# Performance work log

Measured on AMD Instinct MI355X. Metric: run time of the kernel, lower is better.

Reference implementation:

```python
import jax, jax.numpy as jnp
import numpy as np

NS, NP, EJ, ER = 10000, 2048, 32768, 32768  # skills, job/resume pairs, edges
D, H = 1536, 8
NEG_SLOPE_ATT = 0.2   # GAT attention leaky_relu
NEG_SLOPE = 0.01      # F.leaky_relu / nn.LeakyReLU default


def setup_inputs() -> dict:
    key = jax.random.key(0)
    ks = jax.random.split(key, 20)
    rn = lambda k, shp, s=1.0: jax.random.normal(k, shp, dtype=jnp.float32) * s
    s_d = 1.0 / np.sqrt(D)
    return {
        "x_skill": rn(ks[0], (NS, D)),
        "x_job": rn(ks[1], (NP, D)),
        "x_resume": rn(ks[2], (NP, D)),
        # GraphConv params (lin_rel has bias, lin_root bias=False in PyG)
        "W_rel": rn(ks[3], (D, D), s_d),
        "b_rel": jnp.zeros((D,), jnp.float32),
        "W_root": rn(ks[4], (D, D), s_d),
        # GATConv params (heads=8, concat=False)
        "W_gat_src": rn(ks[5], (D, H * D), s_d),
        "W_gat_dst": rn(ks[6], (D, H * D), s_d),
        "att_src": rn(ks[7], (H, D), s_d),
        "att_dst": rn(ks[8], (H, D), s_d),
        "b_gat": jnp.zeros((D,), jnp.float32),
        # MLP: [3072 -> 512 -> 128 -> 1]
        "W1": rn(ks[9], (2 * D, 512), 1.0 / np.sqrt(2 * D)),
        "b1": jnp.zeros((512,), jnp.float32),
        "W2": rn(ks[10], (512, 128), 1.0 / np.sqrt(512)),
        "b2": jnp.zeros((128,), jnp.float32),
        "W3": rn(ks[11], (128, 1), 1.0 / np.sqrt(128)),
        "b3": jnp.zeros((1,), jnp.float32),
        # edge lists (src = skill idx, dst = job/resume idx)
        "edge_src_job": jax.random.randint(ks[12], (EJ,), 0, NS, dtype=jnp.int32),
        "edge_dst_job": jax.random.randint(ks[13], (EJ,), 0, NP, dtype=jnp.int32),
        "edge_src_res": jax.random.randint(ks[14], (ER,), 0, NS, dtype=jnp.int32),
        "edge_dst_res": jax.random.randint(ks[15], (ER,), 0, NP, dtype=jnp.int32),
    }


def reference(x_skill, x_job, x_resume, W_rel, b_rel, W_root,
              W_gat_src, W_gat_dst, att_src, att_dst, b_gat,
              W1, b1, W2, b2, W3, b3,
              edge_src_job, edge_dst_job, edge_src_res, edge_dst_res):
    n_pair = x_job.shape[0]

    # --- GraphConv (skill -> job): sum-aggregate then linear + root ---
    agg = jax.ops.segment_sum(x_skill[edge_src_job], edge_dst_job,
                              num_segments=n_pair)                  # [NP, D]
    h_job = agg @ W_rel + b_rel + x_job @ W_root                     # [NP, D]

    # --- GATConv (skill -> resume), heads=H, concat=False, no self-loops ---
    xs = (x_skill @ W_gat_src).reshape(-1, H, D)                     # [NS, H, D]
    xd = (x_resume @ W_gat_dst).reshape(-1, H, D)                    # [NP, H, D]
    a_src = jnp.einsum('nhd,hd->nh', xs, att_src)                    # [NS, H]
    a_dst = jnp.einsum('nhd,hd->nh', xd, att_dst)                    # [NP, H]
    e = jax.nn.leaky_relu(a_src[edge_src_res] + a_dst[edge_dst_res],
                          NEG_SLOPE_ATT)                             # [E, H]
    # segment softmax over edges grouped by destination resume node
    e_max = jax.ops.segment_max(e, edge_dst_res, num_segments=n_pair)
    e_exp = jnp.exp(e - e_max[edge_dst_res])
    denom = jax.ops.segment_sum(e_exp, edge_dst_res, num_segments=n_pair)
    alpha = e_exp / (denom[edge_dst_res] + 1e-16)                    # [E, H]
    msg = xs[edge_src_res] * alpha[:, :, None]                       # [E, H, D]
    out = jax.ops.segment_sum(msg, edge_dst_res, num_segments=n_pair)  # [NP, H, D]
    h_res = out.mean(axis=1) + b_gat                                 # concat=False -> head mean

    # --- combine + MLP ---
    h = jnp.concatenate([jax.nn.leaky_relu(h_job, NEG_SLOPE),
                         jax.nn.leaky_relu(h_res, NEG_SLOPE)], axis=1)  # [NP, 2D]
    h = jax.nn.leaky_relu(h @ W1 + b1, NEG_SLOPE)
    h = jax.nn.leaky_relu(h @ W2 + b2, NEG_SLOPE)
    score = (h @ W3 + b3).squeeze(-1)                                # [NP]
    return score, alpha
```

## Files before the change

### kernel.cpp

```cpp
#include <hip/hip_runtime.h>

#define D_ 1536
#define H_ 8

typedef __attribute__((ext_vector_type(8))) short bf16x8;
typedef __attribute__((ext_vector_type(4))) float f32x4;

__device__ __forceinline__ unsigned short f2bf(float f) {
    unsigned u = __builtin_bit_cast(unsigned, f);
    unsigned r = (u + 0x7fffu + ((u >> 16) & 1u)) >> 16;
    return (unsigned short)r;
}

__device__ __forceinline__ unsigned pack2bf(float a, float b) {
    return (unsigned)f2bf(a) | ((unsigned)f2bf(b) << 16);
}

__device__ __forceinline__ float bflo(unsigned u) { return __builtin_bit_cast(float, u << 16); }
__device__ __forceinline__ float bfhi(unsigned u) { return __builtin_bit_cast(float, u & 0xffff0000u); }

__device__ __forceinline__ void gload16(const void* g, void* l) {
    __builtin_amdgcn_global_load_lds((const __attribute__((address_space(1))) void*)g,
                                     (__attribute__((address_space(3))) void*)l, 16, 0, 0);
}

__global__ __launch_bounds__(256) void k_vmat(const float* __restrict__ Wsrc,
                                              const float* __restrict__ Wdst,
                                              const float* __restrict__ att_s,
                                              const float* __restrict__ att_d,
                                              float* __restrict__ Vsrc,
                                              float* __restrict__ Vdst) {
    int id = blockIdx.x;
    int sel = id >= (D_ * H_);
    int idx = sel ? id - D_ * H_ : id;
    int d = idx >> 3, h = idx & 7;
    const float* W = (sel ? Wdst : Wsrc) + (size_t)d * (H_ * D_) + (size_t)h * D_;
    const float* at = (sel ? att_d : att_s) + (size_t)h * D_;
    float s = 0.f;
    for (int i = threadIdx.x; i < D_; i += 256) s += W[i] * at[i];
    for (int o = 32; o; o >>= 1) s += __shfl_down(s, o);
    __shared__ float red[4];
    if ((threadIdx.x & 63) == 0) red[threadIdx.x >> 6] = s;
    __syncthreads();
    if (threadIdx.x == 0) (sel ? Vdst : Vsrc)[d * H_ + h] = red[0] + red[1] + red[2] + red[3];
}

__global__ __launch_bounds__(256) void k_a(const float* __restrict__ x,
                                           const float* __restrict__ V,
                                           float* __restrict__ out, int N) {
    int n = blockIdx.x;
    if (n >= N) return;
    float part[H_] = {};
    const float* xr = x + (size_t)n * D_;
    #pragma unroll
    for (int j = 0; j < 6; j++) {
        int d = threadIdx.x + j * 256;
        float xv = xr[d];
        const float* vp = V + d * H_;
        #pragma unroll
        for (int h = 0; h < H_; h++) part[h] += xv * vp[h];
    }
    __shared__ float red[4][H_];
    int lane = threadIdx.x & 63, w = threadIdx.x >> 6;
    #pragma unroll
    for (int h = 0; h < H_; h++) {
        float v = part[h];
        for (int o = 32; o; o >>= 1) v += __shfl_down(v, o);
        if (lane == 0) red[w][h] = v;
    }
    __syncthreads();
    if (threadIdx.x < H_)
        out[(size_t)n * H_ + threadIdx.x] =
            red[0][threadIdx.x] + red[1][threadIdx.x] + red[2][threadIdx.x] + red[3][threadIdx.x];
}

__global__ void k_count(const int* __restrict__ dj, int ej, const int* __restrict__ dr, int er,
                        int* cnt_j, int* cnt_r) {
    int i = blockIdx.x * blockDim.x + threadIdx.x;
    if (i < ej) atomicAdd(&cnt_j[dj[i]], 1);
    else if (i < ej + er) atomicAdd(&cnt_r[dr[i - ej]], 1);
}

__global__ void k_scan(const int* __restrict__ cnt_j, int* off_j,
                       const int* __restrict__ cnt_r, int* off_r, int NP) {
    const int* cnt = blockIdx.x ? cnt_r : cnt_j;
    int* off = blockIdx.x ? off_r : off_j;
    int lane = threadIdx.x;
    int chunk = (NP + 63) / 64;
    int base = lane * chunk;
    int sum = 0;
    for (int i = 0; i < chunk; i++) { int idx = base + i; if (idx < NP) sum += cnt[idx]; }
    int incl = sum;
    for (int o = 1; o < 64; o <<= 1) { int t = __shfl_up(incl, o); if (lane >= o) incl += t; }
    int run = incl - sum;
    for (int i = 0; i < chunk; i++) { int idx = base + i; if (idx < NP) { off[idx] = run; run += cnt[idx]; } }
    if (lane == 63) off[NP] = run;
}

__global__ void k_scatter(const int* __restrict__ dj, int ej, const int* __restrict__ dr, int er,
                          const int* __restrict__ off_j, int* fill_j, int* sid_j,
                          const int* __restrict__ off_r, int* fill_r, int* sid_r) {
    int i = blockIdx.x * blockDim.x + threadIdx.x;
    if (i < ej) {
        int p = dj[i];
        int slot = atomicAdd(&fill_j[p], 1);
        sid_j[off_j[p] + slot] = i;
    } else if (i < ej + er) {
        int e = i - ej;
        int p = dr[e];
        int slot = atomicAdd(&fill_r[p], 1);
        sid_r[off_r[p] + slot] = e;
    }
}

__global__ __launch_bounds__(256) void k_xsb(const float* __restrict__ x, unsigned* __restrict__ xb) {
    int p = blockIdx.x;
    const float2* xr = (const float2*)x + (size_t)p * 768 + threadIdx.x;
    unsigned* o = xb + (size_t)p * 768 + threadIdx.x;
    #pragma unroll
    for (int j = 0; j < 3; j++) { float2 v = xr[j * 256]; o[j * 256] = pack2bf(v.x, v.y); }
}

__global__ __launch_bounds__(256) void k_agg(const unsigned* __restrict__ xb, const int* __restrict__ src,
                                             const int* __restrict__ sid, const int* __restrict__ cnt,
                                             const int* __restrict__ off, unsigned* __restrict__ cat_u) {
    int p = blockIdx.x;
    int n = cnt[p], o = off[p];
    float2 acc[3] = {};
    int i = 0;
    for (; i + 2 <= n; i += 2) {
        int e0 = sid[o + i], e1 = sid[o + i + 1];
        const unsigned* r0 = xb + (size_t)src[e0] * 768 + threadIdx.x;
        const unsigned* r1 = xb + (size_t)src[e1] * 768 + threadIdx.x;
        unsigned v0[3], v1[3];
        #pragma unroll
        for (int j = 0; j < 3; j++) { v0[j] = r0[j * 256]; v1[j] = r1[j * 256]; }
        #pragma unroll
        for (int j = 0; j < 3; j++) {
            acc[j].x += bflo(v0[j]) + bflo(v1[j]);
            acc[j].y += bfhi(v0[j]) + bfhi(v1[j]);
        }
    }
    if (i < n) {
        int e0 = sid[o + i];
        const unsigned* r0 = xb + (size_t)src[e0] * 768 + threadIdx.x;
        #pragma unroll
        for (int j = 0; j < 3; j++) { unsigned v = r0[j * 256]; acc[j].x += bflo(v); acc[j].y += bfhi(v); }
    }
    unsigned* orow = cat_u + (size_t)p * 1536 + threadIdx.x;
    #pragma unroll
    for (int j = 0; j < 3; j++) orow[j * 256] = pack2bf(acc[j].x, acc[j].y);
}

__global__ __launch_bounds__(256) void k_xjob(const float* __restrict__ x_job,
                                              unsigned* __restrict__ cat_u) {
    int p = blockIdx.x;
    const float2* xr = (const float2*)x_job + (size_t)p * 768 + threadIdx.x;
    unsigned* orow = cat_u + (size_t)p * 1536 + 768 + threadIdx.x;
    #pragma unroll
    for (int j = 0; j < 3; j++) { float2 v = xr[j * 256]; orow[j * 256] = pack2bf(v.x, v.y); }
}

__global__ void k_softmax(const float* __restrict__ a_src, const float* __restrict__ a_dst,
                          const int* __restrict__ src, const int* __restrict__ sid,
                          const int* __restrict__ cnt, const int* __restrict__ off,
                          float* __restrict__ alpha_out) {
    int p = blockIdx.x;
    int n = cnt[p], o = off[p];
    if (n == 0) return;
    int lane = threadIdx.x;
    #pragma unroll 1
    for (int h = 0; h < H_; h++) {
        float ad = a_dst[(size_t)p * H_ + h];
        float m = -3.4e38f;
        for (int i = lane; i < n; i += 64) {
            int e = sid[o + i];
            float v = a_src[(size_t)src[e] * H_ + h] + ad;
            v = v >= 0.f ? v : 0.2f * v;
            m = fmaxf(m, v);
        }
        for (int o2 = 32; o2; o2 >>= 1) m = fmaxf(m, __shfl_xor(m, o2));
        float s = 0.f;
        for (int i = lane; i < n; i += 64) {
            int e = sid[o + i];
            float v = a_src[(size_t)src[e] * H_ + h] + ad;
            v = v >= 0.f ? v : 0.2f * v;
            s += expf(v - m);
        }
        for (int o2 = 32; o2; o2 >>= 1) s += __shfl_xor(s, o2);
        float inv = 1.f / (s + 1e-16f);
        for (int i = lane; i < n; i += 64) {
            int e = sid[o + i];
            float v = a_src[(size_t)src[e] * H_ + h] + ad;
            v = v >= 0.f ? v : 0.2f * v;
            alpha_out[(size_t)e * H_ + h] = expf(v - m) * inv;
        }
    }
}

__global__ __launch_bounds__(256) void k_aggatt(const unsigned* __restrict__ xb,
                                                const float* __restrict__ alpha,
                                                const int* __restrict__ src, const int* __restrict__ sid,
                                                const int* __restrict__ cnt, const int* __restrict__ off,
                                                unsigned* __restrict__ aggatt_u) {
    int p = blockIdx.x;
    int n = cnt[p], o = off[p];
    float2 acc[H_][3] = {};
    int i = 0;
    for (; i + 2 <= n; i += 2) {
        int e0 = sid[o + i], e1 = sid[o + i + 1];
        const unsigned* r0 = xb + (size_t)src[e0] * 768 + threadIdx.x;
        const unsigned* r1 = xb + (size_t)src[e1] * 768 + threadIdx.x;
        unsigned v0[3], v1[3];
        #pragma unroll
        for (int j = 0; j < 3; j++) { v0[j] = r0[j * 256]; v1[j] = r1[j * 256]; }
        const float* a0 = alpha + (size_t)e0 * H_;
        const float* a1 = alpha + (size_t)e1 * H_;
        float f0[3][2], f1[3][2];
        #pragma unroll
        for (int j = 0; j < 3; j++) {
            f0[j][0] = bflo(v0[j]); f0[j][1] = bfhi(v0[j]);
            f1[j][0] = bflo(v1[j]); f1[j][1] = bfhi(v1[j]);
        }
        #pragma unroll
        for (int h = 0; h < H_; h++) {
            float w0 = a0[h], w1 = a1[h];
            #pragma unroll
            for (int j = 0; j < 3; j++) {
                acc[h][j].x += w0 * f0[j][0] + w1 * f1[j][0];
                acc[h][j].y += w0 * f0[j][1] + w1 * f1[j][1];
            }
        }
    }
    if (i < n) {
        int e0 = sid[o + i];
        const unsigned* r0 = xb + (size_t)src[e0] * 768 + threadIdx.x;
        unsigned v0[3];
        #pragma unroll
        for (int j = 0; j < 3; j++) v0[j] = r0[j * 256];
        const float* a0 = alpha + (size_t)e0 * H_;
        #pragma unroll
        for (int h = 0; h < H_; h++) {
            float w0 = a0[h];
            #pragma unroll
            for (int j = 0; j < 3; j++) {
                acc[h][j].x += w0 * bflo(v0[j]);
                acc[h][j].y += w0 * bfhi(v0[j]);
            }
        }
    }
    unsigned* orow = aggatt_u + (size_t)p * (H_ * 768) + threadIdx.x;
    #pragma unroll
    for (int h = 0; h < H_; h++)
        #pragma unroll
        for (int j = 0; j < 3; j++)
            orow[h * 768 + j * 256] = pack2bf(acc[h][j].x, acc[h][j].y);
}

template <int GATB>
__global__ __launch_bounds__(256) void k_tr(const float* __restrict__ in, int ldin,
                                            unsigned short* __restrict__ out, int ldout) {
    __shared__ float t[64][65];
    int k0 = blockIdx.y * 64, n0 = blockIdx.x * 64;
    int tx = threadIdx.x & 63, ty = threadIdx.x >> 6;
    #pragma unroll
    for (int i = 0; i < 16; i++) {
        int k = k0 + ty + i * 4;
        const float* rp;
        if (GATB) {
            int d2 = k % D_, h = k / D_;
            rp = in + (size_t)d2 * (H_ * D_) + (size_t)h * D_;
        } else {
            rp = in + (size_t)k * ldin;
        }
        t[ty + i * 4][tx] = rp[n0 + tx];
    }
    __syncthreads();
    int tx2 = threadIdx.x & 31, ty2 = threadIdx.x >> 5;
    #pragma unroll
    for (int i = 0; i < 8; i++) {
        int nl = ty2 + i * 8;
        unsigned v = pack2bf(t[tx2 * 2][nl], t[tx2 * 2 + 1][nl]);
        *(unsigned*)(out + (size_t)(n0 + nl) * ldout + k0 + tx2 * 2) = v;
    }
}

__global__ __launch_bounds__(512, 4) void gemm_sk(const unsigned short* __restrict__ A, int lda,
                                                  const unsigned short* __restrict__ BT, int ldb,
                                                  float* __restrict__ P, int N, int bs, int extra) {
    __shared__ unsigned short As[2][256 * 32];
    __shared__ unsigned short Bs[2][128 * 32];
    int tid = threadIdx.x;
    int lane = tid & 63, wid = tid >> 6;

    int nwg = gridDim.x * gridDim.y;
    int bidh = blockIdx.y * gridDim.x + blockIdx.x;
    int swz = (bidh & 7) * (nwg >> 3) + (bidh >> 3);
    int bn = (swz % gridDim.x) * 128;
    int bm = (swz / gridDim.x) * 256;

    int z = blockIdx.z;
    int steps = bs + (z < extra);
    int kb = z * bs + min(z, extra);
    int kbase = kb * 32, kend = kbase + steps * 32;

    int wr = wid >> 1, wc = wid & 1;
    int fr = lane & 15, g = lane >> 4;

    int ra0 = tid >> 2, sa0 = tid & 3;
    int ra1 = (tid + 512) >> 2, sa1 = tid & 3;
    int sg_a0 = sa0 ^ ((ra0 >> 1) & 3);
    int sg_a1 = sa1 ^ ((ra1 >> 1) & 3);
    int sg_b = sa0 ^ ((ra0 >> 1) & 3);

    f32x4 acc[4][4] = {};

    auto stage = [&](int buf, int k0) {
        gload16(A + (size_t)(bm + ra0) * lda + k0 + sg_a0 * 8, &As[buf][tid * 8]);
        gload16(A + (size_t)(bm + ra1) * lda + k0 + sg_a1 * 8, &As[buf][(tid + 512) * 8]);
        gload16(BT + (size_t)(bn + ra0) * ldb + k0 + sg_b * 8, &Bs[buf][tid * 8]);
    };

    stage(0, kbase);
    int cur = 0;
    for (int k0 = kbase; k0 < kend; k0 += 32) {
        if (k0 + 32 < kend) {
            stage(cur ^ 1, k0 + 32);
            asm volatile("s_waitcnt vmcnt(3)" ::: "memory");
        } else {
            asm volatile("s_waitcnt vmcnt(0)" ::: "memory");
        }
        __builtin_amdgcn_s_barrier();
        __builtin_amdgcn_sched_barrier(0);
        bf16x8 a[4], b[4];
        #pragma unroll
        for (int mi = 0; mi < 4; mi++) {
            int row = wr * 64 + mi * 16 + fr;
            a[mi] = *(const bf16x8*)(&As[cur][row * 32 + ((g ^ ((row >> 1) & 3)) * 8)]);
        }
        #pragma unroll
        for (int ni = 0; ni < 4; ni++) {
            int row = wc * 64 + ni * 16 + fr;
            b[ni] = *(const bf16x8*)(&Bs[cur][row * 32 + ((g ^ ((row >> 1) & 3)) * 8)]);
        }
        __builtin_amdgcn_s_setprio(1);
        #pragma unroll
        for (int mi = 0; mi < 4; mi++)
            #pragma unroll
            for (int ni = 0; ni < 4; ni++)
                acc[mi][ni] = __builtin_amdgcn_mfma_f32_16x16x32_bf16(a[mi], b[ni], acc[mi][ni], 0, 0, 0);
        __builtin_amdgcn_s_setprio(0);
        __builtin_amdgcn_s_barrier();
        __builtin_amdgcn_sched_barrier(0);
        cur ^= 1;
    }

    size_t MN = (size_t)N * (size_t)(gridDim.y * 256);
    float* Pz = P + (size_t)z * MN;
    #pragma unroll
    for (int mi = 0; mi < 4; mi++) {
        int r0 = bm + wr * 64 + mi * 16 + (lane >> 4) * 4;
        #pragma unroll
        for (int ni = 0; ni < 4; ni++) {
            int c = bn + wc * 64 + ni * 16 + (lane & 15);
            #pragma unroll
            for (int j = 0; j < 4; j++)
                Pz[(size_t)(r0 + j) * N + c] = acc[mi][ni][j];
        }
    }
}

template <int OUT_BF16>
__global__ __launch_bounds__(256) void k_reduce(const float* __restrict__ P, int S, int MN, int N,
                                                void* __restrict__ Cout, int ldc,
                                                const float* __restrict__ bias, float scale,
                                                int useLeaky) {
    int idx = (blockIdx.x * 256 + threadIdx.x) * 4;
    if (idx >= MN) return;
    float4 v = *(const float4*)(P + idx);
    for (int s = 1; s < S; s++) {
        float4 t = *(const float4*)(P + (size_t)s * MN + idx);
        v.x += t.x; v.y += t.y; v.z += t.z; v.w += t.w;
    }
    int m = idx / N, n = idx - m * N;
    float vv[4] = {v.x, v.y, v.z, v.w};
    #pragma unroll
    for (int j = 0; j < 4; j++) {
        float x = vv[j] * scale + bias[n + j];
        if (useLeaky) x = x >= 0.f ? x : 0.01f * x;
        if (OUT_BF16) ((unsigned short*)Cout)[(size_t)m * ldc + n + j] = f2bf(x);
        else ((float*)Cout)[(size_t)m * ldc + n + j] = x;
    }
}

__global__ void k_score(const float* __restrict__ h2, const float* __restrict__ W3,
                        const float* __restrict__ b3, float* __restrict__ out) {
    int p = blockIdx.x;
    int lane = threadIdx.x;
    const float* r = h2 + (size_t)p * 128;
    float s = r[lane] * W3[lane] + r[lane + 64] * W3[lane + 64];
    for (int o = 32; o; o >>= 1) s += __shfl_down(s, o);
    if (lane == 0) out[p] = s + b3[0];
}

extern "C" void kernel_launch(void* const* d_in, const int* in_sizes, int n_in,
                              void* d_out, int out_size, void* d_ws, size_t ws_size,
                              hipStream_t stream) {
    const float* x_skill = (const float*)d_in[0];
    const float* x_job   = (const float*)d_in[1];
    const float* x_resume= (const float*)d_in[2];
    const float* W_rel   = (const float*)d_in[3];
    const float* b_rel   = (const float*)d_in[4];
    const float* W_root  = (const float*)d_in[5];
    const float* W_gs    = (const float*)d_in[6];
    const float* W_gd    = (const float*)d_in[7];
    const float* att_s   = (const float*)d_in[8];
    const float* att_d   = (const float*)d_in[9];
    const float* b_gat   = (const float*)d_in[10];
    const float* W1      = (const float*)d_in[11];
    const float* b1      = (const float*)d_in[12];
    const float* W2      = (const float*)d_in[13];
    const float* b2      = (const float*)d_in[14];
    const float* W3      = (const float*)d_in[15];
    const float* b3      = (const float*)d_in[16];
    const int* esj = (const int*)d_in[17];
    const int* edj = (const int*)d_in[18];
    const int* esr = (const int*)d_in[19];
    const int* edr = (const int*)d_in[20];

    const int NS = in_sizes[0] / D_;
    const int NP = in_sizes[1] / D_;
    const int EJ = in_sizes[17];
    const int ER = in_sizes[19];

    float* score = (float*)d_out;
    float* alpha = score + NP;

    char* ws = (char*)d_ws;
    size_t off = 0;
    auto alloc = [&](size_t bytes) -> void* {
        void* p = ws + off;
        off = (off + bytes + 255) & ~(size_t)255;
        return p;
    };

    int* cnt_j  = (int*)alloc((size_t)4 * NP * sizeof(int));
    int* fill_j = cnt_j + NP;
    int* cnt_r  = cnt_j + 2 * NP;
    int* fill_r = cnt_j + 3 * NP;
    int* off_j  = (int*)alloc((size_t)(NP + 1) * sizeof(int));
    int* off_r  = (int*)alloc((size_t)(NP + 1) * sizeof(int));
    int* sid_j  = (int*)alloc((size_t)EJ * sizeof(int));
    int* sid_r  = (int*)alloc((size_t)ER * sizeof(int));
    float* Vsrc = (float*)alloc((size_t)D_ * H_ * 4);
    float* Vdst = (float*)alloc((size_t)D_ * H_ * 4);
    float* a_src= (float*)alloc((size_t)NS * H_ * 4);
    float* a_dst= (float*)alloc((size_t)NP * H_ * 4);
    unsigned short* cat_in = (unsigned short*)alloc((size_t)NP * 2 * D_ * 2);
    unsigned short* aggatt = (unsigned short*)alloc((size_t)NP * H_ * D_ * 2);
    unsigned short* BT1    = (unsigned short*)alloc((size_t)D_ * 2 * D_ * 2);
    unsigned short* BTg    = (unsigned short*)alloc((size_t)D_ * H_ * D_ * 2);
    unsigned short* BTw1   = (unsigned short*)alloc((size_t)512 * 2 * D_ * 2);
    unsigned short* BTw2   = (unsigned short*)alloc((size_t)128 * 512 * 2);
    unsigned short* hcat   = (unsigned short*)alloc((size_t)NP * 2 * D_ * 2);
    unsigned short* h1b    = (unsigned short*)alloc((size_t)NP * 512 * 2);
    float* h2   = (float*)alloc((size_t)NP * 128 * 4);
    float* Pbuf = (float*)alloc((size_t)16 * NP * 512 * 4);
    unsigned* xsb = (unsigned*)Pbuf;

    hipMemsetAsync(cnt_j, 0, (size_t)4 * NP * sizeof(int), stream);

    k_tr<0><<<dim3(D_ / 64, D_ / 64), 256, 0, stream>>>(W_rel, D_, BT1, 2 * D_);
    k_tr<0><<<dim3(D_ / 64, D_ / 64), 256, 0, stream>>>(W_root, D_, BT1 + D_, 2 * D_);
    k_tr<1><<<dim3(D_ / 64, (H_ * D_) / 64), 256, 0, stream>>>(W_gs, 0, BTg, H_ * D_);
    k_tr<0><<<dim3(512 / 64, (2 * D_) / 64), 256, 0, stream>>>(W1, 512, BTw1, 2 * D_);
    k_tr<0><<<dim3(128 / 64, 512 / 64), 256, 0, stream>>>(W2, 128, BTw2, 512);

    k_xsb<<<NS, 256, 0, stream>>>(x_skill, xsb);
    k_vmat<<<2 * D_ * H_, 256, 0, stream>>>(W_gs, W_gd, att_s, att_d, Vsrc, Vdst);
    k_a<<<NS, 256, 0, stream>>>(x_skill, Vsrc, a_src, NS);
    k_a<<<NP, 256, 0, stream>>>(x_resume, Vdst, a_dst, NP);

    int egrid = (EJ + ER + 255) / 256;
    k_count<<<egrid, 256, 0, stream>>>(edj, EJ, edr, ER, cnt_j, cnt_r);
    k_scan<<<2, 64, 0, stream>>>(cnt_j, off_j, cnt_r, off_r, NP);
    k_scatter<<<egrid, 256, 0, stream>>>(edj, EJ, edr, ER, off_j, fill_j, sid_j, off_r, fill_r, sid_r);

    k_agg<<<NP, 256, 0, stream>>>(xsb, esj, sid_j, cnt_j, off_j, (unsigned*)cat_in);
    k_xjob<<<NP, 256, 0, stream>>>(x_job, (unsigned*)cat_in);
    k_softmax<<<NP, 64, 0, stream>>>(a_src, a_dst, esr, sid_r, cnt_r, off_r, alpha);
    k_aggatt<<<NP, 256, 0, stream>>>(xsb, alpha, esr, sid_r, cnt_r, off_r, (unsigned*)aggatt);

    const int MN_f = NP * D_;
    const int MN_1 = NP * 512;
    const int MN_2 = NP * 128;

    gemm_sk<<<dim3(D_ / 128, NP / 256, 5), 512, 0, stream>>>(
        cat_in, 2 * D_, BT1, 2 * D_, Pbuf, D_, 19, 1);
    k_reduce<1><<<MN_f / 1024, 256, 0, stream>>>(Pbuf, 5, MN_f, D_, hcat, 2 * D_, b_rel, 1.f, 1);

    gemm_sk<<<dim3(D_ / 128, NP / 256, 5), 512, 0, stream>>>(
        aggatt, H_ * D_, BTg, H_ * D_, Pbuf, D_, 76, 4);
    k_reduce<1><<<MN_f / 1024, 256, 0, stream>>>(Pbuf, 5, MN_f, D_, hcat + D_, 2 * D_, b_gat, 1.f / H_, 1);

    gemm_sk<<<dim3(512 / 128, NP / 256, 16), 512, 0, stream>>>(
        hcat, 2 * D_, BTw1, 2 * D_, Pbuf, 512, 6, 0);
    k_reduce<1><<<MN_1 / 1024, 256, 0, stream>>>(Pbuf, 16, MN_1, 512, h1b, 512, b1, 1.f, 1);

    gemm_sk<<<dim3(128 / 128, NP / 256, 16), 512, 0, stream>>>(
        h1b, 512, BTw2, 512, Pbuf, 128, 1, 0);
    k_reduce<0><<<MN_2 / 1024, 256, 0, stream>>>(Pbuf, 16, MN_2, 128, h2, 128, b2, 1.f, 1);

    k_score<<<NP, 64, 0, stream>>>(h2, W3, b3, score);
}
```

Measured before the change: 452.1 us.

## Fuse preprocessing kernels, triple-buffer GEMM, and fuse final MLP layers

```diff
diff --git a/kernel.cpp b/kernel.cpp
--- a/kernel.cpp
+++ b/kernel.cpp
@@ -24,25 +24,73 @@
                                      (__attribute__((address_space(3))) void*)l, 16, 0, 0);
 }
 
-__global__ __launch_bounds__(256) void k_vmat(const float* __restrict__ Wsrc,
-                                              const float* __restrict__ Wdst,
-                                              const float* __restrict__ att_s,
-                                              const float* __restrict__ att_d,
-                                              float* __restrict__ Vsrc,
-                                              float* __restrict__ Vdst) {
+__global__ __launch_bounds__(256) void k_vmat2(const float* __restrict__ Wsrc,
+                                               const float* __restrict__ Wdst,
+                                               const float* __restrict__ att_s,
+                                               const float* __restrict__ att_d,
+                                               float* __restrict__ Vsrc,
+                                               float* __restrict__ Vdst) {
     int id = blockIdx.x;
-    int sel = id >= (D_ * H_);
-    int idx = sel ? id - D_ * H_ : id;
-    int d = idx >> 3, h = idx & 7;
-    const float* W = (sel ? Wdst : Wsrc) + (size_t)d * (H_ * D_) + (size_t)h * D_;
-    const float* at = (sel ? att_d : att_s) + (size_t)h * D_;
-    float s = 0.f;
-    for (int i = threadIdx.x; i < D_; i += 256) s += W[i] * at[i];
-    for (int o = 32; o; o >>= 1) s += __shfl_down(s, o);
-    __shared__ float red[4];
-    if ((threadIdx.x & 63) == 0) red[threadIdx.x >> 6] = s;
+    int sel = id >= D_;
+    int d = sel ? id - D_ : id;
+    const float4* wr = (const float4*)((sel ? Wdst : Wsrc) + (size_t)d * (H_ * D_));
+    const float* at = sel ? att_d : att_s;
+    int t = threadIdx.x;
+    float part[H_];
+    #pragma unroll
+    for (int h = 0; h < H_; h++) {
+        const float4* ar = (const float4*)(at + h * D_);
+        float4 w0 = wr[h * 384 + t];
+        float4 a0 = ar[t];
+        float s = w0.x * a0.x + w0.y * a0.y + w0.z * a0.z + w0.w * a0.w;
+        if (t < 128) {
+            float4 w1 = wr[h * 384 + 256 + t];
+            float4 a1 = ar[256 + t];
+            s += w1.x * a1.x + w1.y * a1.y + w1.z * a1.z + w1.w * a1.w;
+        }
+        part[h] = s;
+    }
+    __shared__ float red[4][H_];
+    int lane = t & 63, w = t >> 6;
+    #pragma unroll
+    for (int h = 0; h < H_; h++) {
+        float v = part[h];
+        for (int o = 32; o; o >>= 1) v += __shfl_down(v, o);
+        if (lane == 0) red[w][h] = v;
+    }
     __syncthreads();
-    if (threadIdx.x == 0) (sel ? Vdst : Vsrc)[d * H_ + h] = red[0] + red[1] + red[2] + red[3];
+    if (t < H_) (sel ? Vdst : Vsrc)[d * H_ + t] = red[0][t] + red[1][t] + red[2][t] + red[3][t];
+}
+
+__global__ __launch_bounds__(256) void k_a_xsb(const float* __restrict__ x,
+                                               const float* __restrict__ V,
+                                               float* __restrict__ out,
+                                               unsigned* __restrict__ xb) {
+    int n = blockIdx.x;
+    float part[H_] = {};
+    const float2* xr = (const float2*)x + (size_t)n * 768;
+    unsigned* ob = xb + (size_t)n * 768;
+    #pragma unroll
+    for (int j = 0; j < 3; j++) {
+        int e = threadIdx.x + j * 256;
+        float2 v = xr[e];
+        ob[e] = pack2bf(v.x, v.y);
+        const float* vp = V + (size_t)(2 * e) * H_;
+        #pragma unroll
+        for (int h = 0; h < H_; h++) part[h] += v.x * vp[h] + v.y * vp[h + H_];
+    }
+    __shared__ float red[4][H_];
+    int lane = threadIdx.x & 63, w = threadIdx.x >> 6;
+    #pragma unroll
+    for (int h = 0; h < H_; h++) {
+        float v = part[h];
+        for (int o = 32; o; o >>= 1) v += __shfl_down(v, o);
+        if (lane == 0) red[w][h] = v;
+    }
+    __syncthreads();
+    if (threadIdx.x < H_)
+        out[(size_t)n * H_ + threadIdx.x] =
+            red[0][threadIdx.x] + red[1][threadIdx.x] + red[2][threadIdx.x] + red[3][threadIdx.x];
 }
 
 __global__ __launch_bounds__(256) void k_a(const float* __restrict__ x,
@@ -113,17 +161,11 @@
     }
 }
 
-__global__ __launch_bounds__(256) void k_xsb(const float* __restrict__ x, unsigned* __restrict__ xb) {
-    int p = blockIdx.x;
-    const float2* xr = (const float2*)x + (size_t)p * 768 + threadIdx.x;
-    unsigned* o = xb + (size_t)p * 768 + threadIdx.x;
-    #pragma unroll
-    for (int j = 0; j < 3; j++) { float2 v = xr[j * 256]; o[j * 256] = pack2bf(v.x, v.y); }
-}
-
 __global__ __launch_bounds__(256) void k_agg(const unsigned* __restrict__ xb, const int* __restrict__ src,
                                              const int* __restrict__ sid, const int* __restrict__ cnt,
-                                             const int* __restrict__ off, unsigned* __restrict__ cat_u) {
+                                             const int* __restrict__ off,
+                                             const float* __restrict__ x_job,
+                                             unsigned* __restrict__ cat_u) {
     int p = blockIdx.x;
     int n = cnt[p], o = off[p];
     float2 acc[3] = {};
@@ -150,15 +192,9 @@
     unsigned* orow = cat_u + (size_t)p * 1536 + threadIdx.x;
     #pragma unroll
     for (int j = 0; j < 3; j++) orow[j * 256] = pack2bf(acc[j].x, acc[j].y);
-}
-
-__global__ __launch_bounds__(256) void k_xjob(const float* __restrict__ x_job,
-                                              unsigned* __restrict__ cat_u) {
-    int p = blockIdx.x;
-    const float2* xr = (const float2*)x_job + (size_t)p * 768 + threadIdx.x;
-    unsigned* orow = cat_u + (size_t)p * 1536 + 768 + threadIdx.x;
-    #pragma unroll
-    for (int j = 0; j < 3; j++) { float2 v = xr[j * 256]; orow[j * 256] = pack2bf(v.x, v.y); }
+    const float2* xjr = (const float2*)x_job + (size_t)p * 768 + threadIdx.x;
+    #pragma unroll
+    for (int j = 0; j < 3; j++) { float2 v = xjr[j * 256]; orow[768 + j * 256] = pack2bf(v.x, v.y); }
 }
 
 __global__ void k_softmax(const float* __restrict__ a_src, const float* __restrict__ a_dst,
@@ -288,8 +324,8 @@
 __global__ __launch_bounds__(512, 4) void gemm_sk(const unsigned short* __restrict__ A, int lda,
                                                   const unsigned short* __restrict__ BT, int ldb,
                                                   float* __restrict__ P, int N, int bs, int extra) {
-    __shared__ unsigned short As[2][256 * 32];
-    __shared__ unsigned short Bs[2][128 * 32];
+    __shared__ unsigned short As[3][256 * 32];
+    __shared__ unsigned short Bs[3][128 * 32];
     int tid = threadIdx.x;
     int lane = tid & 63, wid = tid >> 6;
 
@@ -300,18 +336,18 @@
     int bm = (swz / gridDim.x) * 256;
 
     int z = blockIdx.z;
-    int steps = bs + (z < extra);
+    int nt = bs + (z < extra);
     int kb = z * bs + min(z, extra);
-    int kbase = kb * 32, kend = kbase + steps * 32;
+    int kbase = kb * 32;
 
     int wr = wid >> 1, wc = wid & 1;
     int fr = lane & 15, g = lane >> 4;
 
     int ra0 = tid >> 2, sa0 = tid & 3;
-    int ra1 = (tid + 512) >> 2, sa1 = tid & 3;
+    int ra1 = (tid + 512) >> 2;
     int sg_a0 = sa0 ^ ((ra0 >> 1) & 3);
-    int sg_a1 = sa1 ^ ((ra1 >> 1) & 3);
-    int sg_b = sa0 ^ ((ra0 >> 1) & 3);
+    int sg_a1 = sa0 ^ ((ra1 >> 1) & 3);
+    int sg_b = sg_a0;
 
     f32x4 acc[4][4] = {};
 
@@ -322,16 +358,19 @@
     };
 
     stage(0, kbase);
-    int cur = 0;
-    for (int k0 = kbase; k0 < kend; k0 += 32) {
-        if (k0 + 32 < kend) {
-            stage(cur ^ 1, k0 + 32);
+    if (nt > 1) stage(1, kbase + 32);
+    for (int t = 0; t < nt; t++) {
+        if (t + 2 < nt) {
+            stage((t + 2) % 3, kbase + (t + 2) * 32);
+            asm volatile("s_waitcnt vmcnt(6)" ::: "memory");
+        } else if (t + 1 < nt) {
             asm volatile("s_waitcnt vmcnt(3)" ::: "memory");
         } else {
             asm volatile("s_waitcnt vmcnt(0)" ::: "memory");
         }
         __builtin_amdgcn_s_barrier();
         __builtin_amdgcn_sched_barrier(0);
+        int cur = t % 3;
         bf16x8 a[4], b[4];
         #pragma unroll
         for (int mi = 0; mi < 4; mi++) {
@@ -352,7 +391,6 @@
         __builtin_amdgcn_s_setprio(0);
         __builtin_amdgcn_s_barrier();
         __builtin_amdgcn_sched_barrier(0);
-        cur ^= 1;
     }
 
     size_t MN = (size_t)N * (size_t)(gridDim.y * 256);
@@ -393,14 +431,56 @@
     }
 }
 
-__global__ void k_score(const float* __restrict__ h2, const float* __restrict__ W3,
-                        const float* __restrict__ b3, float* __restrict__ out) {
-    int p = blockIdx.x;
-    int lane = threadIdx.x;
-    const float* r = h2 + (size_t)p * 128;
-    float s = r[lane] * W3[lane] + r[lane + 64] * W3[lane + 64];
-    for (int o = 32; o; o >>= 1) s += __shfl_down(s, o);
-    if (lane == 0) out[p] = s + b3[0];
+__global__ __launch_bounds__(256) void k_mlp2(const unsigned short* __restrict__ h1b,
+                                              const float* __restrict__ W2,
+                                              const float* __restrict__ b2,
+                                              const float* __restrict__ W3,
+                                              const float* __restrict__ b3,
+                                              float* __restrict__ score) {
+    __shared__ unsigned h1s[8][256];
+    __shared__ float red[4][4];
+    int p0 = blockIdx.x * 8;
+    int tid = threadIdx.x;
+    const unsigned* hsrc = (const unsigned*)h1b + (size_t)p0 * 256;
+    #pragma unroll
+    for (int i = 0; i < 8; i++) {
+        int idx = tid + i * 256;
+        h1s[idx >> 8][idx & 255] = hsrc[idx];
+    }
+    __syncthreads();
+    int c = tid & 127, rg = tid >> 7;
+    float acc[4] = {};
+    for (int k = 0; k < 512; k += 2) {
+        float w0 = W2[(size_t)k * 128 + c];
+        float w1 = W2[(size_t)(k + 1) * 128 + c];
+        #pragma unroll
+        for (int r = 0; r < 4; r++) {
+            unsigned hv = h1s[rg * 4 + r][k >> 1];
+            acc[r] += bflo(hv) * w0 + bfhi(hv) * w1;
+        }
+    }
+    float w3 = W3[c];
+    float pr[4];
+    #pragma unroll
+    for (int r = 0; r < 4; r++) {
+        float v = acc[r] + b2[c];
+        v = v >= 0.f ? v : 0.01f * v;
+        pr[r] = v * w3;
+    }
+    #pragma unroll
+    for (int r = 0; r < 4; r++)
+        for (int o = 32; o; o >>= 1) pr[r] += __shfl_down(pr[r], o);
+    int w = tid >> 6;
+    if ((tid & 63) == 0) {
+        #pragma unroll
+        for (int r = 0; r < 4; r++) red[w][r] = pr[r];
+    }
+    __syncthreads();
+    if (tid < 8) {
+        int rg2 = tid >> 2, r = tid & 3;
+        float s = red[rg2 * 2][r] + red[rg2 * 2 + 1][r] + b3[0];
+        score[p0 + rg2 * 4 + r] = s;
+    }
 }
 
 extern "C" void kernel_launch(void* const* d_in, const int* in_sizes, int n_in,
@@ -461,11 +541,9 @@
     unsigned short* BT1    = (unsigned short*)alloc((size_t)D_ * 2 * D_ * 2);
     unsigned short* BTg    = (unsigned short*)alloc((size_t)D_ * H_ * D_ * 2);
     unsigned short* BTw1   = (unsigned short*)alloc((size_t)512 * 2 * D_ * 2);
-    unsigned short* BTw2   = (unsigned short*)alloc((size_t)128 * 512 * 2);
     unsigned short* hcat   = (unsigned short*)alloc((size_t)NP * 2 * D_ * 2);
     unsigned short* h1b    = (unsigned short*)alloc((size_t)NP * 512 * 2);
-    float* h2   = (float*)alloc((size_t)NP * 128 * 4);
-    float* Pbuf = (float*)alloc((size_t)16 * NP * 512 * 4);
+    float* Pbuf = (float*)alloc((size_t)5 * NP * D_ * 4);
     unsigned* xsb = (unsigned*)Pbuf;
 
     hipMemsetAsync(cnt_j, 0, (size_t)4 * NP * sizeof(int), stream);
@@ -474,11 +552,9 @@
     k_tr<0><<<dim3(D_ / 64, D_ / 64), 256, 0, stream>>>(W_root, D_, BT1 + D_, 2 * D_);
     k_tr<1><<<dim3(D_ / 64, (H_ * D_) / 64), 256, 0, stream>>>(W_gs, 0, BTg, H_ * D_);
     k_tr<0><<<dim3(512 / 64, (2 * D_) / 64), 256, 0, stream>>>(W1, 512, BTw1, 2 * D_);
-    k_tr<0><<<dim3(128 / 64, 512 / 64), 256, 0, stream>>>(W2, 128, BTw2, 512);
-
-    k_xsb<<<NS, 256, 0, stream>>>(x_skill, xsb);
-    k_vmat<<<2 * D_ * H_, 256, 0, stream>>>(W_gs, W_gd, att_s, att_d, Vsrc, Vdst);
-    k_a<<<NS, 256, 0, stream>>>(x_skill, Vsrc, a_src, NS);
+
+    k_vmat2<<<2 * D_, 256, 0, stream>>>(W_gs, W_gd, att_s, att_d, Vsrc, Vdst);
+    k_a_xsb<<<NS, 256, 0, stream>>>(x_skill, Vsrc, a_src, xsb);
     k_a<<<NP, 256, 0, stream>>>(x_resume, Vdst, a_dst, NP);
 
     int egrid = (EJ + ER + 255) / 256;
@@ -486,14 +562,12 @@
     k_scan<<<2, 64, 0, stream>>>(cnt_j, off_j, cnt_r, off_r, NP);
     k_scatter<<<egrid, 256, 0, stream>>>(edj, EJ, edr, ER, off_j, fill_j, sid_j, off_r, fill_r, sid_r);
 
-    k_agg<<<NP, 256, 0, stream>>>(xsb, esj, sid_j, cnt_j, off_j, (unsigned*)cat_in);
-    k_xjob<<<NP, 256, 0, stream>>>(x_job, (unsigned*)cat_in);
+    k_agg<<<NP, 256, 0, stream>>>(xsb, esj, sid_j, cnt_j, off_j, x_job, (unsigned*)cat_in);
     k_softmax<<<NP, 64, 0, stream>>>(a_src, a_dst, esr, sid_r, cnt_r, off_r, alpha);
     k_aggatt<<<NP, 256, 0, stream>>>(xsb, alpha, esr, sid_r, cnt_r, off_r, (unsigned*)aggatt);
 
     const int MN_f = NP * D_;
     const int MN_1 = NP * 512;
-    const int MN_2 = NP * 128;
 
     gemm_sk<<<dim3(D_ / 128, NP / 256, 5), 512, 0, stream>>>(
         cat_in, 2 * D_, BT1, 2 * D_, Pbuf, D_, 19, 1);
@@ -503,13 +577,9 @@
         aggatt, H_ * D_, BTg, H_ * D_, Pbuf, D_, 76, 4);
     k_reduce<1><<<MN_f / 1024, 256, 0, stream>>>(Pbuf, 5, MN_f, D_, hcat + D_, 2 * D_, b_gat, 1.f / H_, 1);
 
-    gemm_sk<<<dim3(512 / 128, NP / 256, 16), 512, 0, stream>>>(
-        hcat, 2 * D_, BTw1, 2 * D_, Pbuf, 512, 6, 0);
-    k_reduce<1><<<MN_1 / 1024, 256, 0, stream>>>(Pbuf, 16, MN_1, 512, h1b, 512, b1, 1.f, 1);
-
-    gemm_sk<<<dim3(128 / 128, NP / 256, 16), 512, 0, stream>>>(
-        h1b, 512, BTw2, 512, Pbuf, 128, 1, 0);
-    k_reduce<0><<<MN_2 / 1024, 256, 0, stream>>>(Pbuf, 16, MN_2, 128, h2, 128, b2, 1.f, 1);
-
-    k_score<<<NP, 64, 0, stream>>>(h2, W3, b3, score);
-}
+    gemm_sk<<<dim3(512 / 128, NP / 256, 8), 512, 0, stream>>>(
+        hcat, 2 * D_, BTw1, 2 * D_, Pbuf, 512, 12, 0);
+    k_reduce<1><<<MN_1 / 1024, 256, 0, stream>>>(Pbuf, 8, MN_1, 512, h1b, 512, b1, 1.f, 1);
+
+    k_mlp2<<<NP / 8, 256, 0, stream>>>(h1b, W2, b2, W3, b3, score);
+}
```

Result: no change. 449.0 us (-0.7%).
